# Kernel tuning notes

Hardware: AMD Instinct MI355X
Metric: run time of the kernel (lower is better)

The kernel has to match this reference:

```python
import jax, jax.numpy as jnp
import numpy as np

L, H, P = 8192, 512, 512


def setup_inputs() -> dict:
    key = jax.random.key(0)
    ks = jax.random.split(key, 7)
    u = jax.random.normal(ks[0], (L, H), dtype=jnp.float32)
    # diagonal continuous-time state matrix Lambda = Lambda_re + i*Lambda_im (stable: Re < 0)
    Lambda_re = -0.5 * jax.random.uniform(ks[1], (P,), dtype=jnp.float32) - 0.1
    Lambda_im = jnp.pi * jax.random.normal(ks[2], (P,), dtype=jnp.float32)
    # B_tilde (P,H) and C_tilde (H,P) parameterized as real/imag pairs (..., 2)
    B = jax.random.normal(ks[3], (P, H, 2), dtype=jnp.float32) / np.sqrt(2.0 * H)
    C = jax.random.normal(ks[4], (H, P, 2), dtype=jnp.float32) / np.sqrt(2.0 * P)
    D = jax.random.normal(ks[5], (H,), dtype=jnp.float32)
    log_step = jax.random.uniform(ks[6], (P,), dtype=jnp.float32,
                                  minval=np.log(1e-3), maxval=np.log(1e-1))
    return {"u": u, "Lambda_re": Lambda_re, "Lambda_im": Lambda_im,
            "B": B, "C": C, "D": D, "log_step": log_step}


def _binop(qi, qj):
    # binary operator for parallel scan of diagonal linear recurrence
    A_i, Bu_i = qi
    A_j, Bu_j = qj
    return (A_j * A_i, A_j * Bu_i + Bu_j)


def reference(u, Lambda_re, Lambda_im, B, C, D, log_step):
    Lambda = (Lambda_re + 1j * Lambda_im).astype(jnp.complex64)          # (P,)
    B_tilde = (B[..., 0] + 1j * B[..., 1]).astype(jnp.complex64)         # (P,H)
    C_tilde = (C[..., 0] + 1j * C[..., 1]).astype(jnp.complex64)         # (H,P)
    Delta = jnp.exp(log_step)                                            # (P,)
    # zero-order-hold discretization
    Lambda_bar = jnp.exp(Lambda * Delta)                                 # (P,)
    B_bar = ((Lambda_bar - 1.0) / Lambda)[:, None] * B_tilde             # (P,H)
    # Bu_t = B_bar @ u_t for all t  -> (L,P)
    Bu = jnp.einsum('lh,ph->lp', u.astype(jnp.complex64), B_bar)
    A_elems = jnp.broadcast_to(Lambda_bar, (u.shape[0], P))              # (L,P)
    _, xs = jax.lax.associative_scan(_binop, (A_elems, Bu), axis=0)      # (L,P) states
    # y_t = Re(C_tilde @ x_t) + D * u_t
    y = jnp.einsum('lp,hp->lh', xs, C_tilde).real + D * u
    return y
```

## Files before the change

### kernel.cpp

```cpp
#include <hip/hip_runtime.h>
#include <hip/hip_bf16.h>

#define L_DIM 8192
#define H_DIM 512
#define P_DIM 512
#define CHUNK 32
#define NCHUNK (L_DIM / CHUNK)

typedef __attribute__((ext_vector_type(8))) short bf16x8;
typedef __attribute__((ext_vector_type(4))) float f32x4;

__device__ inline short f2bf(float x) {
    union { float f; unsigned u; } v; v.f = x;
    unsigned r = v.u + 0x7fffu + ((v.u >> 16) & 1u);
    return (short)(r >> 16);
}
__device__ inline float bflo2f(unsigned w) {
    union { unsigned u; float f; } v; v.u = w << 16; return v.f;
}
__device__ inline float bfhi2f(unsigned w) {
    union { unsigned u; float f; } v; v.u = w & 0xffff0000u; return v.f;
}

__device__ inline void gload_lds16(const void* g, void* l) {
    __builtin_amdgcn_global_load_lds(
        (const __attribute__((address_space(1))) unsigned int*)g,
        (__attribute__((address_space(3))) unsigned int*)l, 16, 0, 0);
}

template<int N> __device__ inline void waitcnt_vm() {
    if constexpr (N == 0)       asm volatile("s_waitcnt vmcnt(0)" ::: "memory");
    else if constexpr (N == 3)  asm volatile("s_waitcnt vmcnt(3)" ::: "memory");
    else if constexpr (N == 4)  asm volatile("s_waitcnt vmcnt(4)" ::: "memory");
    else if constexpr (N == 6)  asm volatile("s_waitcnt vmcnt(6)" ::: "memory");
    else if constexpr (N == 8)  asm volatile("s_waitcnt vmcnt(8)" ::: "memory");
}

__global__ __launch_bounds__(256) void k_prep(
        const float* __restrict__ Lre, const float* __restrict__ Lim,
        const float* __restrict__ Bin, const float* __restrict__ log_step,
        const float* __restrict__ Cin, const float* __restrict__ u,
        short* __restrict__ Bcat, short* __restrict__ Ccat,
        short* __restrict__ u_bf,
        float* __restrict__ lambda_bar, float* __restrict__ lambda_powN) {
    const int blk = blockIdx.x;
    const int tid = threadIdx.x;
    if (blk < P_DIM) {
        int p = blk;
        float lr = Lre[p], li = Lim[p];
        float dt = expf(log_step[p]);
        float ar = lr * dt, ai = li * dt;
        float er = expf(ar);
        float lbr = er * cosf(ai);
        float lbi = er * sinf(ai);
        float nr = lbr - 1.0f, ni = lbi;
        float den = lr * lr + li * li;
        float fr = (nr * lr + ni * li) / den;
        float fi = (ni * lr - nr * li) / den;
        if (tid == 0) {
            lambda_bar[2 * p] = lbr;
            lambda_bar[2 * p + 1] = lbi;
            float eN = expf(ar * (float)CHUNK);
            lambda_powN[2 * p] = eN * cosf(ai * (float)CHUNK);
            lambda_powN[2 * p + 1] = eN * sinf(ai * (float)CHUNK);
        }
        for (int h = tid; h < H_DIM; h += 256) {
            float br = Bin[((size_t)p * H_DIM + h) * 2 + 0];
            float bi = Bin[((size_t)p * H_DIM + h) * 2 + 1];
            Bcat[(size_t)(2 * p) * H_DIM + h] = f2bf(fr * br - fi * bi);
            Bcat[(size_t)(2 * p + 1) * H_DIM + h] = f2bf(fr * bi + fi * br);
        }
    } else if (blk < P_DIM + 1024) {
        int idx = (blk - P_DIM) * 256 + tid;
        int h = idx >> 9, p = idx & 511;
        float cr = Cin[(size_t)idx * 2 + 0];
        float ci = Cin[(size_t)idx * 2 + 1];
        Ccat[(size_t)h * (2 * P_DIM) + 2 * p + 0] = f2bf(cr);
        Ccat[(size_t)h * (2 * P_DIM) + 2 * p + 1] = f2bf(-ci);
    } else {
        int i = (blk - P_DIM - 1024) * 256 + tid;
        const float4* uf = (const float4*)u;
        float4 a0 = uf[(size_t)i * 2];
        float4 a1 = uf[(size_t)i * 2 + 1];
        bf16x8 sv;
        sv[0] = f2bf(a0.x); sv[1] = f2bf(a0.y); sv[2] = f2bf(a0.z); sv[3] = f2bf(a0.w);
        sv[4] = f2bf(a1.x); sv[5] = f2bf(a1.y); sv[6] = f2bf(a1.z); sv[7] = f2bf(a1.w);
        *(bf16x8*)&u_bf[(size_t)i * 8] = sv;
    }
}

template<int BM, int BN, bool OBF16, bool EPI, bool SUMM>
__global__ __launch_bounds__(256) void k_gemm(
        const short* __restrict__ A, const short* __restrict__ B,
        void* __restrict__ Cout, int M, int N, int K, int nwgn,
        const float* __restrict__ Dv, const short* __restrict__ Ubf,
        const float* __restrict__ Lamb, float* __restrict__ S) {
    constexpr int MF = BM / 32;
    constexpr int NF = BN / 32;
    constexpr int APL = BM / 64;
    constexpr int BPL = BN / 64;
    constexpr int LPS = APL + BPL;
    constexpr int ASZ = BM * 32 * 2;
    constexpr int BSZ = BN * 32 * 2;
    constexpr int STG = 3 * (ASZ + BSZ);
    constexpr int TILE = BM * 272;
    constexpr int SMEM_SZ = STG > TILE ? STG : TILE;
    __shared__ __align__(16) char smem[SMEM_SZ];

    const int tid = threadIdx.x;
    const int lane = tid & 63;
    const int wid = tid >> 6;
    const int wr = wid >> 1, wc = wid & 1;

    const int nwg = gridDim.x;
    const int orig = blockIdx.x;
    const int id = (orig & 7) * (nwg >> 3) + (orig >> 3);
    const int bm = (id / nwgn) * BM;
    const int bn = (id % nwgn) * BN;

    f32x4 acc[MF][NF] = {};
    const int arow = wr * (BM / 2) + (lane & 15);
    const int brow = wc * (BN / 2) + (lane & 15);
    const int rslot = (((lane >> 4) ^ (lane & 3) ^ ((lane >> 2) & 3)) << 4);

    auto stage = [&](int buf, int kk) {
#pragma unroll
        for (int q = 0; q < APL; ++q) {
            int sb = q * 4096 + tid * 16;
            int row = sb >> 6, slot = (sb >> 4) & 3;
            int gs = slot ^ ((row ^ (row >> 2)) & 3);
            const char* src = (const char*)A + ((size_t)(bm + row) * K + kk) * 2 + gs * 16;
            gload_lds16(src, smem + buf * ASZ + sb);
        }
#pragma unroll
        for (int q = 0; q < BPL; ++q) {
            int sb = q * 4096 + tid * 16;
            int row = sb >> 6, slot = (sb >> 4) & 3;
            int gs = slot ^ ((row ^ (row >> 2)) & 3);
            const char* src = (const char*)B + ((size_t)(bn + row) * K + kk) * 2 + gs * 16;
            gload_lds16(src, smem + 3 * ASZ + buf * BSZ + sb);
        }
    };

    const int nt = K >> 5;
    stage(0, 0);
    if (nt > 1) stage(1, 32);
    waitcnt_vm<LPS>();
    __builtin_amdgcn_s_barrier();
    __builtin_amdgcn_sched_barrier(0);

    for (int t = 0; t < nt; ++t) {
        const int cb = t % 3;
        const char* Ab = smem + cb * ASZ;
        const char* Bb = smem + 3 * ASZ + cb * BSZ;
        bf16x8 af[MF], bfr[NF];
#pragma unroll
        for (int m = 0; m < MF; ++m)
            af[m] = *(const bf16x8*)(Ab + (arow + m * 16) * 64 + rslot);
#pragma unroll
        for (int n = 0; n < NF; ++n)
            bfr[n] = *(const bf16x8*)(Bb + (brow + n * 16) * 64 + rslot);
        if (t + 2 < nt) stage((t + 2) % 3, (t + 2) * 32);
        __builtin_amdgcn_s_setprio(1);
#pragma unroll
        for (int m = 0; m < MF; ++m)
#pragma unroll
            for (int n = 0; n < NF; ++n)
                acc[m][n] = __builtin_amdgcn_mfma_f32_16x16x32_bf16(af[m], bfr[n], acc[m][n], 0, 0, 0);
        __builtin_amdgcn_s_setprio(0);
        if (t + 1 < nt) {
            if (t + 2 < nt) waitcnt_vm<LPS>(); else waitcnt_vm<0>();
            __builtin_amdgcn_s_barrier();
            __builtin_amdgcn_sched_barrier(0);
        }
    }

    __syncthreads();
    const int fq = lane >> 4, fr = lane & 15;

    if (OBF16) {
#pragma unroll
        for (int m = 0; m < MF; ++m)
#pragma unroll
            for (int n = 0; n < NF; ++n) {
                int rowL = wr * (BM / 2) + m * 16 + fq * 4;
                int colL = wc * (BN / 2) + n * 16 + fr;
#pragma unroll
                for (int j = 0; j < 4; ++j)
                    *(short*)(smem + (rowL + j) * 272 + colL * 2) = f2bf(acc[m][n][j]);
            }
        __syncthreads();
        constexpr int SEGS = BN / 8;
#pragma unroll
        for (int it = 0; it < (BM * SEGS) / 256; ++it) {
            int f = it * 256 + tid;
            int row = f / SEGS, seg = f % SEGS;
            uint4 v = *(const uint4*)(smem + row * 272 + seg * 16);
            *(uint4*)((short*)Cout + (size_t)(bm + row) * N + bn + seg * 8) = v;
        }
        if (SUMM) {
            constexpr int CH = BN / 2;
            constexpr int NCH = BM / CHUNK;
            if (tid < CH * NCH) {
                const int c_loc = tid / CH;
                const int ch = tid % CH;
                const int gch = (bn >> 1) + ch;
                const float lr = Lamb[2 * gch], li = Lamb[2 * gch + 1];
                float xr = 0.f, xi = 0.f;
#pragma unroll 8
                for (int j = 0; j < CHUNK; ++j) {
                    unsigned wv = *(const unsigned*)(smem + (c_loc * CHUNK + j) * 272 + ch * 4);
                    float br = bflo2f(wv), bi = bfhi2f(wv);
                    float nxr = lr * xr - li * xi + br;
                    float nxi = lr * xi + li * xr + bi;
                    xr = nxr; xi = nxi;
                }
                ((float2*)S)[(size_t)((bm >> 5) + c_loc) * P_DIM + gch] = make_float2(xr, xi);
            }
        }
    } else {
#pragma unroll
        for (int m = 0; m < MF; ++m)
#pragma unroll
            for (int n = 0; n < NF; ++n) {
                int rowL = wr * (BM / 2) + m * 16 + fq * 4;
                int colL = wc * (BN / 2) + n * 16 + fr;
#pragma unroll
                for (int j = 0; j < 4; ++j)
                    *(float*)(smem + (rowL + j) * 272 + colL * 4) = acc[m][n][j];
            }
        __syncthreads();
        constexpr int SEGS = BN / 4;
#pragma unroll
        for (int it = 0; it < (BM * SEGS) / 256; ++it) {
            int f = it * 256 + tid;
            int row = f / SEGS, seg = f % SEGS;
            float4 v = *(const float4*)(smem + row * 272 + seg * 16);
            int gr = bm + row, gc = bn + seg * 4;
            if (EPI) {
                const short* up = Ubf + (size_t)gr * N + gc;
                short4 us = *(const short4*)up;
                float4 dv = *(const float4*)(Dv + gc);
                v.x += dv.x * bflo2f((unsigned)(unsigned short)us.x);
                v.y += dv.y * bflo2f((unsigned)(unsigned short)us.y);
                v.z += dv.z * bflo2f((unsigned)(unsigned short)us.z);
                v.w += dv.w * bflo2f((unsigned)(unsigned short)us.w);
            }
            *(float4*)((float*)Cout + (size_t)gr * N + gc) = v;
        }
    }
}

__global__ __launch_bounds__(64) void k_scan_combine(const float* __restrict__ S,
                                                     const float* __restrict__ lambda_powN,
                                                     float* __restrict__ pref) {
    const int ch = blockIdx.x * 64 + threadIdx.x;
    const float lNr = lambda_powN[2 * ch], lNi = lambda_powN[2 * ch + 1];
    const float2* Sp = (const float2*)S;
    float2* Pp = (float2*)pref;
    float2 curb[16], nxtb[16];
#pragma unroll
    for (int j = 0; j < 16; ++j) curb[j] = Sp[(size_t)j * P_DIM + ch];
    float xr = 0.f, xi = 0.f;
    for (int c0 = 0; c0 < NCHUNK; c0 += 16) {
        if (c0 + 16 < NCHUNK) {
#pragma unroll
            for (int j = 0; j < 16; ++j) nxtb[j] = Sp[(size_t)(c0 + 16 + j) * P_DIM + ch];
        }
#pragma unroll
        for (int j = 0; j < 16; ++j) {
            Pp[(size_t)(c0 + j) * P_DIM + ch] = make_float2(xr, xi);
            float nxr = lNr * xr - lNi * xi + curb[j].x;
            float nxi = lNr * xi + lNi * xr + curb[j].y;
            xr = nxr; xi = nxi;
        }
#pragma unroll
        for (int j = 0; j < 16; ++j) curb[j] = nxtb[j];
    }
}

__global__ __launch_bounds__(256) void k_scan_apply(const unsigned* __restrict__ Bu,
                                                    unsigned* __restrict__ XsB,
                                                    const float* __restrict__ lambda_bar,
                                                    const float* __restrict__ pref) {
    int gid = blockIdx.x * blockDim.x + threadIdx.x;
    int c = gid >> 9, p = gid & 511;
    const float lr = lambda_bar[2 * p], li = lambda_bar[2 * p + 1];
    float2 x0 = ((const float2*)pref)[(size_t)c * P_DIM + p];
    float xr = x0.x, xi = x0.y;
    const unsigned* bu = Bu + (size_t)c * CHUNK * P_DIM + p;
#pragma unroll 4
    for (int j = 0; j < CHUNK; ++j) {
        unsigned w = bu[(size_t)j * P_DIM];
        float br = bflo2f(w), bi = bfhi2f(w);
        float nxr = lr * xr - li * xi + br;
        float nxi = lr * xi + li * xr + bi;
        xr = nxr; xi = nxi;
        unsigned pk = (unsigned)(unsigned short)f2bf(xr)
                    | ((unsigned)(unsigned short)f2bf(xi) << 16);
        XsB[((size_t)c * CHUNK + j) * P_DIM + p] = pk;
    }
}

extern "C" void kernel_launch(void* const* d_in, const int* in_sizes, int n_in,
                              void* d_out, int out_size, void* d_ws, size_t ws_size,
                              hipStream_t stream) {
    const float* u        = (const float*)d_in[0];
    const float* Lre      = (const float*)d_in[1];
    const float* Lim      = (const float*)d_in[2];
    const float* Bin      = (const float*)d_in[3];
    const float* Cin      = (const float*)d_in[4];
    const float* Dv       = (const float*)d_in[5];
    const float* log_step = (const float*)d_in[6];
    float* y = (float*)d_out;

    char* w = (char*)d_ws;
    size_t off = 0;
    short* Bcat = (short*)(w + off); off += (size_t)2 * P_DIM * H_DIM * 2;
    short* Ccat = (short*)(w + off); off += (size_t)2 * P_DIM * H_DIM * 2;
    float* lamb = (float*)(w + off); off += 2 * P_DIM * 4;
    float* lamN = (float*)(w + off); off += 2 * P_DIM * 4;
    float* S    = (float*)(w + off); off += (size_t)NCHUNK * 2 * P_DIM * 4;
    float* pref = (float*)(w + off); off += (size_t)NCHUNK * 2 * P_DIM * 4;
    unsigned* Bu  = (unsigned*)(w + off); off += (size_t)L_DIM * P_DIM * 4;
    unsigned* XsB = (unsigned*)(w + off); off += (size_t)L_DIM * P_DIM * 4;
    short* u_bf   = (short*)(w + off);   off += (size_t)L_DIM * H_DIM * 2;

    k_prep<<<P_DIM + 1024 + 2048, 256, 0, stream>>>(
        Lre, Lim, Bin, log_step, Cin, u, Bcat, Ccat, u_bf, lamb, lamN);
    k_gemm<128, 128, true, false, true><<<(L_DIM / 128) * ((2 * P_DIM) / 128), 256, 0, stream>>>(
        u_bf, Bcat, (void*)Bu, L_DIM, 2 * P_DIM, H_DIM, (2 * P_DIM) / 128,
        nullptr, nullptr, lamb, S);
    k_scan_combine<<<8, 64, 0, stream>>>(S, lamN, pref);
    k_scan_apply<<<(NCHUNK * P_DIM) / 256, 256, 0, stream>>>(Bu, XsB, lamb, pref);
    k_gemm<128, 64, false, true, false><<<(L_DIM / 128) * (H_DIM / 64), 256, 0, stream>>>(
        (const short*)XsB, Ccat, (void*)y, L_DIM, H_DIM, 2 * P_DIM, H_DIM / 64,
        Dv, u_bf, nullptr, nullptr);
}
```

Measured before the change: 68.39 us.

## Fuse scan combine, scan apply and output GEMM into one cooperative kernel

Replaces the three kernels for chunk-prefix combine, per-chunk scan apply and the output GEMM with a single cooperative kernel of 512 blocks that uses grid-wide syncs between phases. The first GEMM is specialized into a non-template kernel. The intent is to remove kernel launch gaps and tail effects between these small dependent stages. The cost is that the serial combine runs on only 2 blocks while the other blocks wait at grid.sync, and the two grid barriers add their own overhead.

```diff
diff --git a/kernel.cpp b/kernel.cpp
--- a/kernel.cpp
+++ b/kernel.cpp
@@ -1,5 +1,8 @@
 #include <hip/hip_runtime.h>
 #include <hip/hip_bf16.h>
+#include <hip/hip_cooperative_groups.h>
+
+namespace cg = cooperative_groups;
 
 #define L_DIM 8192
 #define H_DIM 512
@@ -89,23 +92,18 @@
     }
 }
 
-template<int BM, int BN, bool OBF16, bool EPI, bool SUMM>
-__global__ __launch_bounds__(256) void k_gemm(
+__global__ __launch_bounds__(256) void k_gemm1(
         const short* __restrict__ A, const short* __restrict__ B,
-        void* __restrict__ Cout, int M, int N, int K, int nwgn,
-        const float* __restrict__ Dv, const short* __restrict__ Ubf,
-        const float* __restrict__ Lamb, float* __restrict__ S) {
-    constexpr int MF = BM / 32;
-    constexpr int NF = BN / 32;
-    constexpr int APL = BM / 64;
-    constexpr int BPL = BN / 64;
-    constexpr int LPS = APL + BPL;
+        short* __restrict__ Cout, const float* __restrict__ Lamb,
+        float* __restrict__ S) {
+    constexpr int BM = 128, BN = 128;
+    constexpr int MF = 4, NF = 4;
+    constexpr int APL = 2, BPL = 2, LPS = 4;
     constexpr int ASZ = BM * 32 * 2;
     constexpr int BSZ = BN * 32 * 2;
-    constexpr int STG = 3 * (ASZ + BSZ);
-    constexpr int TILE = BM * 272;
-    constexpr int SMEM_SZ = STG > TILE ? STG : TILE;
-    __shared__ __align__(16) char smem[SMEM_SZ];
+    const int M = L_DIM, N = 2 * P_DIM, K = H_DIM;
+    const int nwgn = N / BN;
+    __shared__ __align__(16) char smem[3 * (ASZ + BSZ)];
 
     const int tid = threadIdx.x;
     const int lane = tid & 63;
@@ -144,7 +142,7 @@
 
     const int nt = K >> 5;
     stage(0, 0);
-    if (nt > 1) stage(1, 32);
+    stage(1, 32);
     waitcnt_vm<LPS>();
     __builtin_amdgcn_s_barrier();
     __builtin_amdgcn_sched_barrier(0);
@@ -177,128 +175,204 @@
 
     __syncthreads();
     const int fq = lane >> 4, fr = lane & 15;
-
-    if (OBF16) {
+#pragma unroll
+    for (int m = 0; m < MF; ++m)
+#pragma unroll
+        for (int n = 0; n < NF; ++n) {
+            int rowL = wr * (BM / 2) + m * 16 + fq * 4;
+            int colL = wc * (BN / 2) + n * 16 + fr;
+#pragma unroll
+            for (int j = 0; j < 4; ++j)
+                *(short*)(smem + (rowL + j) * 272 + colL * 2) = f2bf(acc[m][n][j]);
+        }
+    __syncthreads();
+    constexpr int SEGS = BN / 8;
+#pragma unroll
+    for (int it = 0; it < (BM * SEGS) / 256; ++it) {
+        int f = it * 256 + tid;
+        int row = f / SEGS, seg = f % SEGS;
+        uint4 v = *(const uint4*)(smem + row * 272 + seg * 16);
+        *(uint4*)(Cout + (size_t)(bm + row) * N + bn + seg * 8) = v;
+    }
+    {
+        const int c_loc = tid >> 6;
+        const int ch = tid & 63;
+        const int gch = (bn >> 1) + ch;
+        const float lr = Lamb[2 * gch], li = Lamb[2 * gch + 1];
+        float xr = 0.f, xi = 0.f;
+#pragma unroll 8
+        for (int j = 0; j < CHUNK; ++j) {
+            unsigned wv = *(const unsigned*)(smem + (c_loc * CHUNK + j) * 272 + ch * 4);
+            float br = bflo2f(wv), bi = bfhi2f(wv);
+            float nxr = lr * xr - li * xi + br;
+            float nxi = lr * xi + li * xr + bi;
+            xr = nxr; xi = nxi;
+        }
+        ((float2*)S)[(size_t)((bm >> 5) + c_loc) * P_DIM + gch] = make_float2(xr, xi);
+    }
+}
+
+__global__ __launch_bounds__(256) void k_scan_gemm2(
+        const unsigned* __restrict__ Bu, unsigned* __restrict__ XsB,
+        const float* __restrict__ lamb, const float* __restrict__ lamN,
+        const float* __restrict__ S, float* __restrict__ pref,
+        const short* __restrict__ Ccat, float* __restrict__ y,
+        const float* __restrict__ Dv, const short* __restrict__ u_bf) {
+    constexpr int BM = 128, BN = 64;
+    constexpr int MF = 4, NF = 2;
+    constexpr int APL = 2, BPL = 1, LPS = 3;
+    constexpr int ASZ = BM * 32 * 2;
+    constexpr int BSZ = BN * 32 * 2;
+    __shared__ __align__(16) char smem[3 * (ASZ + BSZ)];
+
+    cg::grid_group grid = cg::this_grid();
+    const int tid = threadIdx.x;
+    const int orig = blockIdx.x;
+    const int nwg = gridDim.x;
+    const int id = (orig & 7) * (nwg >> 3) + (orig >> 3);
+
+    if (orig < 2) {
+        const int ch = orig * 256 + tid;
+        const float lNr = lamN[2 * ch], lNi = lamN[2 * ch + 1];
+        const float2* Sp = (const float2*)S;
+        float2* Pp = (float2*)pref;
+        float2 curb[16], nxtb[16];
+#pragma unroll
+        for (int j = 0; j < 16; ++j) curb[j] = Sp[(size_t)j * P_DIM + ch];
+        float xr = 0.f, xi = 0.f;
+        for (int c0 = 0; c0 < NCHUNK; c0 += 16) {
+            if (c0 + 16 < NCHUNK) {
+#pragma unroll
+                for (int j = 0; j < 16; ++j) nxtb[j] = Sp[(size_t)(c0 + 16 + j) * P_DIM + ch];
+            }
+#pragma unroll
+            for (int j = 0; j < 16; ++j) {
+                Pp[(size_t)(c0 + j) * P_DIM + ch] = make_float2(xr, xi);
+                float nxr = lNr * xr - lNi * xi + curb[j].x;
+                float nxi = lNr * xi + lNi * xr + curb[j].y;
+                xr = nxr; xi = nxi;
+            }
+#pragma unroll
+            for (int j = 0; j < 16; ++j) curb[j] = nxtb[j];
+        }
+    }
+    grid.sync();
+
+    {
+        const int c = (id >> 3) * 4 + ((id & 7) >> 1);
+        const int p = (id & 1) * 256 + tid;
+        const float lr = lamb[2 * p], li = lamb[2 * p + 1];
+        float2 x0 = ((const float2*)pref)[(size_t)c * P_DIM + p];
+        float xr = x0.x, xi = x0.y;
+        const unsigned* bu = Bu + (size_t)c * CHUNK * P_DIM + p;
+#pragma unroll 4
+        for (int j = 0; j < CHUNK; ++j) {
+            unsigned w = bu[(size_t)j * P_DIM];
+            float br = bflo2f(w), bi = bfhi2f(w);
+            float nxr = lr * xr - li * xi + br;
+            float nxi = lr * xi + li * xr + bi;
+            xr = nxr; xi = nxi;
+            unsigned pk = (unsigned)(unsigned short)f2bf(xr)
+                        | ((unsigned)(unsigned short)f2bf(xi) << 16);
+            XsB[((size_t)c * CHUNK + j) * P_DIM + p] = pk;
+        }
+    }
+    grid.sync();
+
+    const short* A = (const short*)XsB;
+    const int M = L_DIM, N = H_DIM, K = 2 * P_DIM;
+    const int nwgn = N / BN;
+    const int lane = tid & 63;
+    const int wid = tid >> 6;
+    const int wr = wid >> 1, wc = wid & 1;
+    const int bm = (id / nwgn) * BM;
+    const int bn = (id % nwgn) * BN;
+
+    f32x4 acc[MF][NF] = {};
+    const int arow = wr * (BM / 2) + (lane & 15);
+    const int brow = wc * (BN / 2) + (lane & 15);
+    const int rslot = (((lane >> 4) ^ (lane & 3) ^ ((lane >> 2) & 3)) << 4);
+
+    auto stage = [&](int buf, int kk) {
+#pragma unroll
+        for (int q = 0; q < APL; ++q) {
+            int sb = q * 4096 + tid * 16;
+            int row = sb >> 6, slot = (sb >> 4) & 3;
+            int gs = slot ^ ((row ^ (row >> 2)) & 3);
+            const char* src = (const char*)A + ((size_t)(bm + row) * K + kk) * 2 + gs * 16;
+            gload_lds16(src, smem + buf * ASZ + sb);
+        }
+#pragma unroll
+        for (int q = 0; q < BPL; ++q) {
+            int sb = q * 4096 + tid * 16;
+            int row = sb >> 6, slot = (sb >> 4) & 3;
+            int gs = slot ^ ((row ^ (row >> 2)) & 3);
+            const char* src = (const char*)Ccat + ((size_t)(bn + row) * K + kk) * 2 + gs * 16;
+            gload_lds16(src, smem + 3 * ASZ + buf * BSZ + sb);
+        }
+    };
+
+    const int nt = K >> 5;
+    stage(0, 0);
+    stage(1, 32);
+    waitcnt_vm<LPS>();
+    __builtin_amdgcn_s_barrier();
+    __builtin_amdgcn_sched_barrier(0);
+
+    for (int t = 0; t < nt; ++t) {
+        const int cb = t % 3;
+        const char* Ab = smem + cb * ASZ;
+        const char* Bb = smem + 3 * ASZ + cb * BSZ;
+        bf16x8 af[MF], bfr[NF];
 #pragma unroll
         for (int m = 0; m < MF; ++m)
-#pragma unroll
-            for (int n = 0; n < NF; ++n) {
-                int rowL = wr * (BM / 2) + m * 16 + fq * 4;
-                int colL = wc * (BN / 2) + n * 16 + fr;
-#pragma unroll
-                for (int j = 0; j < 4; ++j)
-                    *(short*)(smem + (rowL + j) * 272 + colL * 2) = f2bf(acc[m][n][j]);
-            }
-        __syncthreads();
-        constexpr int SEGS = BN / 8;
-#pragma unroll
-        for (int it = 0; it < (BM * SEGS) / 256; ++it) {
-            int f = it * 256 + tid;
-            int row = f / SEGS, seg = f % SEGS;
-            uint4 v = *(const uint4*)(smem + row * 272 + seg * 16);
-            *(uint4*)((short*)Cout + (size_t)(bm + row) * N + bn + seg * 8) = v;
-        }
-        if (SUMM) {
-            constexpr int CH = BN / 2;
-            constexpr int NCH = BM / CHUNK;
-            if (tid < CH * NCH) {
-                const int c_loc = tid / CH;
-                const int ch = tid % CH;
-                const int gch = (bn >> 1) + ch;
-                const float lr = Lamb[2 * gch], li = Lamb[2 * gch + 1];
-                float xr = 0.f, xi = 0.f;
-#pragma unroll 8
-                for (int j = 0; j < CHUNK; ++j) {
-                    unsigned wv = *(const unsigned*)(smem + (c_loc * CHUNK + j) * 272 + ch * 4);
-                    float br = bflo2f(wv), bi = bfhi2f(wv);
-                    float nxr = lr * xr - li * xi + br;
-                    float nxi = lr * xi + li * xr + bi;
-                    xr = nxr; xi = nxi;
-                }
-                ((float2*)S)[(size_t)((bm >> 5) + c_loc) * P_DIM + gch] = make_float2(xr, xi);
-            }
-        }
-    } else {
+            af[m] = *(const bf16x8*)(Ab + (arow + m * 16) * 64 + rslot);
+#pragma unroll
+        for (int n = 0; n < NF; ++n)
+            bfr[n] = *(const bf16x8*)(Bb + (brow + n * 16) * 64 + rslot);
+        if (t + 2 < nt) stage((t + 2) % 3, (t + 2) * 32);
+        __builtin_amdgcn_s_setprio(1);
 #pragma unroll
         for (int m = 0; m < MF; ++m)
 #pragma unroll
-            for (int n = 0; n < NF; ++n) {
-                int rowL = wr * (BM / 2) + m * 16 + fq * 4;
-                int colL = wc * (BN / 2) + n * 16 + fr;
-#pragma unroll
-                for (int j = 0; j < 4; ++j)
-                    *(float*)(smem + (rowL + j) * 272 + colL * 4) = acc[m][n][j];
-            }
-        __syncthreads();
-        constexpr int SEGS = BN / 4;
-#pragma unroll
-        for (int it = 0; it < (BM * SEGS) / 256; ++it) {
-            int f = it * 256 + tid;
-            int row = f / SEGS, seg = f % SEGS;
-            float4 v = *(const float4*)(smem + row * 272 + seg * 16);
-            int gr = bm + row, gc = bn + seg * 4;
-            if (EPI) {
-                const short* up = Ubf + (size_t)gr * N + gc;
-                short4 us = *(const short4*)up;
-                float4 dv = *(const float4*)(Dv + gc);
-                v.x += dv.x * bflo2f((unsigned)(unsigned short)us.x);
-                v.y += dv.y * bflo2f((unsigned)(unsigned short)us.y);
-                v.z += dv.z * bflo2f((unsigned)(unsigned short)us.z);
-                v.w += dv.w * bflo2f((unsigned)(unsigned short)us.w);
-            }
-            *(float4*)((float*)Cout + (size_t)gr * N + gc) = v;
-        }
-    }
-}
-
-__global__ __launch_bounds__(64) void k_scan_combine(const float* __restrict__ S,
-                                                     const float* __restrict__ lambda_powN,
-                                                     float* __restrict__ pref) {
-    const int ch = blockIdx.x * 64 + threadIdx.x;
-    const float lNr = lambda_powN[2 * ch], lNi = lambda_powN[2 * ch + 1];
-    const float2* Sp = (const float2*)S;
-    float2* Pp = (float2*)pref;
-    float2 curb[16], nxtb[16];
-#pragma unroll
-    for (int j = 0; j < 16; ++j) curb[j] = Sp[(size_t)j * P_DIM + ch];
-    float xr = 0.f, xi = 0.f;
-    for (int c0 = 0; c0 < NCHUNK; c0 += 16) {
-        if (c0 + 16 < NCHUNK) {
-#pragma unroll
-            for (int j = 0; j < 16; ++j) nxtb[j] = Sp[(size_t)(c0 + 16 + j) * P_DIM + ch];
-        }
-#pragma unroll
-        for (int j = 0; j < 16; ++j) {
-            Pp[(size_t)(c0 + j) * P_DIM + ch] = make_float2(xr, xi);
-            float nxr = lNr * xr - lNi * xi + curb[j].x;
-            float nxi = lNr * xi + lNi * xr + curb[j].y;
-            xr = nxr; xi = nxi;
-        }
-#pragma unroll
-        for (int j = 0; j < 16; ++j) curb[j] = nxtb[j];
-    }
-}
-
-__global__ __launch_bounds__(256) void k_scan_apply(const unsigned* __restrict__ Bu,
-                                                    unsigned* __restrict__ XsB,
-                                                    const float* __restrict__ lambda_bar,
-                                                    const float* __restrict__ pref) {
-    int gid = blockIdx.x * blockDim.x + threadIdx.x;
-    int c = gid >> 9, p = gid & 511;
-    const float lr = lambda_bar[2 * p], li = lambda_bar[2 * p + 1];
-    float2 x0 = ((const float2*)pref)[(size_t)c * P_DIM + p];
-    float xr = x0.x, xi = x0.y;
-    const unsigned* bu = Bu + (size_t)c * CHUNK * P_DIM + p;
-#pragma unroll 4
-    for (int j = 0; j < CHUNK; ++j) {
-        unsigned w = bu[(size_t)j * P_DIM];
-        float br = bflo2f(w), bi = bfhi2f(w);
-        float nxr = lr * xr - li * xi + br;
-        float nxi = lr * xi + li * xr + bi;
-        xr = nxr; xi = nxi;
-        unsigned pk = (unsigned)(unsigned short)f2bf(xr)
-                    | ((unsigned)(unsigned short)f2bf(xi) << 16);
-        XsB[((size_t)c * CHUNK + j) * P_DIM + p] = pk;
+            for (int n = 0; n < NF; ++n)
+                acc[m][n] = __builtin_amdgcn_mfma_f32_16x16x32_bf16(af[m], bfr[n], acc[m][n], 0, 0, 0);
+        __builtin_amdgcn_s_setprio(0);
+        if (t + 1 < nt) {
+            if (t + 2 < nt) waitcnt_vm<LPS>(); else waitcnt_vm<0>();
+            __builtin_amdgcn_s_barrier();
+            __builtin_amdgcn_sched_barrier(0);
+        }
+    }
+
+    __syncthreads();
+    const int fq = lane >> 4, fr = lane & 15;
+#pragma unroll
+    for (int m = 0; m < MF; ++m)
+#pragma unroll
+        for (int n = 0; n < NF; ++n) {
+            int rowL = wr * (BM / 2) + m * 16 + fq * 4;
+            int colL = wc * (BN / 2) + n * 16 + fr;
+#pragma unroll
+            for (int j = 0; j < 4; ++j)
+                *(float*)(smem + (rowL + j) * 272 + colL * 4) = acc[m][n][j];
+        }
+    __syncthreads();
+    constexpr int SEGS = BN / 4;
+#pragma unroll
+    for (int it = 0; it < (BM * SEGS) / 256; ++it) {
+        int f = it * 256 + tid;
+        int row = f / SEGS, seg = f % SEGS;
+        float4 v = *(const float4*)(smem + row * 272 + seg * 16);
+        int gr = bm + row, gc = bn + seg * 4;
+        const short* up = u_bf + (size_t)gr * N + gc;
+        short4 us = *(const short4*)up;
+        float4 dv = *(const float4*)(Dv + gc);
+        v.x += dv.x * bflo2f((unsigned)(unsigned short)us.x);
+        v.y += dv.y * bflo2f((unsigned)(unsigned short)us.y);
+        v.z += dv.z * bflo2f((unsigned)(unsigned short)us.z);
+        v.w += dv.w * bflo2f((unsigned)(unsigned short)us.w);
+        *(float4*)(y + (size_t)gr * N + gc) = v;
     }
 }
 
@@ -328,12 +402,22 @@
 
     k_prep<<<P_DIM + 1024 + 2048, 256, 0, stream>>>(
         Lre, Lim, Bin, log_step, Cin, u, Bcat, Ccat, u_bf, lamb, lamN);
-    k_gemm<128, 128, true, false, true><<<(L_DIM / 128) * ((2 * P_DIM) / 128), 256, 0, stream>>>(
-        u_bf, Bcat, (void*)Bu, L_DIM, 2 * P_DIM, H_DIM, (2 * P_DIM) / 128,
-        nullptr, nullptr, lamb, S);
-    k_scan_combine<<<8, 64, 0, stream>>>(S, lamN, pref);
-    k_scan_apply<<<(NCHUNK * P_DIM) / 256, 256, 0, stream>>>(Bu, XsB, lamb, pref);
-    k_gemm<128, 64, false, true, false><<<(L_DIM / 128) * (H_DIM / 64), 256, 0, stream>>>(
-        (const short*)XsB, Ccat, (void*)y, L_DIM, H_DIM, 2 * P_DIM, H_DIM / 64,
-        Dv, u_bf, nullptr, nullptr);
-}
+    k_gemm1<<<(L_DIM / 128) * ((2 * P_DIM) / 128), 256, 0, stream>>>(
+        u_bf, Bcat, (short*)Bu, lamb, S);
+    {
+        const unsigned* BuC = Bu;
+        unsigned* XsBp = XsB;
+        const float* lambC = lamb;
+        const float* lamNC = lamN;
+        const float* SC = S;
+        float* prefP = pref;
+        const short* CcatC = Ccat;
+        float* yP = y;
+        const float* DvC = Dv;
+        const short* u_bfC = u_bf;
+        void* kargs[10] = {&BuC, &XsBp, &lambC, &lamNC, &SC, &prefP,
+                           &CcatC, &yP, &DvC, &u_bfC};
+        hipLaunchCooperativeKernel((void*)k_scan_gemm2, dim3(512), dim3(256),
+                                   kargs, 0, stream);
+    }
+}
```

New measurement: 170.4 us. 2.49x slower.
